# Optimization experiments

Hardware: AMD Instinct MI355X
Metric: run time of the kernel (lower is better)

## Reference

```python
import jax, jax.numpy as jnp
import numpy as np

D_IN, D_SAE, T, K = 768, 12288, 64, 64
B = 32


def setup_inputs() -> dict:
    key = jax.random.key(0)
    ks = jax.random.split(key, 4)
    x = jax.random.normal(ks[0], (B, T, D_IN), dtype=jnp.float32)
    W_enc = jax.random.normal(ks[1], (D_IN, D_SAE), dtype=jnp.float32) * (1.0 / D_IN ** 0.5)
    W_dec = jax.random.normal(ks[2], (D_SAE, D_IN), dtype=jnp.float32) * (1.0 / D_SAE ** 0.5)
    b_enc = jnp.zeros((D_SAE,), dtype=jnp.float32)
    b_dec = jnp.zeros((D_IN,), dtype=jnp.float32)
    gate_raw = jnp.zeros((D_SAE,), dtype=jnp.float32)  # gate_init = 0.0 -> sigmoid = 0.5
    return {"x": x, "W_enc": W_enc, "W_dec": W_dec, "b_enc": b_enc,
            "b_dec": b_dec, "gate_raw": gate_raw}


def _topk(pre, k):
    # pre: (B, d_sae) -> sparse (B, d_sae) keeping relu of top-k values per row
    v, i = jax.lax.top_k(pre, k)                      # (B, k)
    z = jnp.zeros_like(pre)
    rows = jnp.arange(pre.shape[0])[:, None]
    return z.at[rows, i].set(jax.nn.relu(v))


def reference(x, W_enc, W_dec, b_enc, b_dec, gate_raw):
    gate = jax.nn.sigmoid(gate_raw)                    # (d_sae,)
    pre_input = jnp.einsum('btd,ds->bts', x, W_enc) + b_enc  # (B, T, d_sae)

    z0 = _topk(pre_input[:, 0, :], K)                  # (B, d_sae)

    def step(z_prev, pre_t):
        z_t = _topk(gate * z_prev + pre_t, K)
        return z_t, z_t

    pre_rest = jnp.swapaxes(pre_input[:, 1:, :], 0, 1)  # (T-1, B, d_sae)
    _, zs = jax.lax.scan(step, z0, pre_rest)            # (T-1, B, d_sae)
    z_seq = jnp.concatenate([z0[:, None, :], jnp.swapaxes(zs, 0, 1)], axis=1)  # (B, T, d_sae)

    x_hat = jnp.einsum('bts,sd->btd', z_seq, W_dec) + b_dec  # (B, T, d_in)
    recon_loss = jnp.mean(jnp.sum((x_hat - x) ** 2, axis=-1))
    return recon_loss, x_hat, z_seq[:, -1, :]
```

## Files before the change

kernel.cpp:

```cpp
#include <hip/hip_runtime.h>
#include <hip/hip_bf16.h>
#include <math.h>

#define D_IN   768
#define D_SAE  12288
#define T_LEN  64
#define K_TOP  64
#define B_SZ   32
#define NROWS  (B_SZ * T_LEN)
#define KT     24

typedef _Float16 h8 __attribute__((ext_vector_type(8)));
typedef float f4 __attribute__((ext_vector_type(4)));

__device__ __forceinline__ unsigned int f2key(float f) {
  unsigned int u = __float_as_uint(f);
  return (u & 0x80000000u) ? ~u : (u | 0x80000000u);
}

__device__ __forceinline__ void barL() {
  __builtin_amdgcn_sched_barrier(0);
  asm volatile("s_waitcnt lgkmcnt(0)" ::: "memory");
  __builtin_amdgcn_s_barrier();
  __builtin_amdgcn_sched_barrier(0);
}

#define GLOAD16(g, l)                                                        \
  __builtin_amdgcn_global_load_lds(                                          \
      (const __attribute__((address_space(1))) unsigned int*)(g),            \
      (__attribute__((address_space(3))) unsigned int*)(l), 16, 0, 0)

__global__ void sae_init_out(float* __restrict__ d_out) {
  int i = blockIdx.x * blockDim.x + threadIdx.x;
  if (i == 0) d_out[0] = 0.0f;
  if (i < B_SZ * D_SAE) d_out[1 + (size_t)NROWS * D_IN + i] = 0.0f;
}

__global__ __launch_bounds__(256) void sae_split_A(
    const float* __restrict__ A, _Float16* __restrict__ Ah, _Float16* __restrict__ Al) {
  int g = blockIdx.x * 256 + threadIdx.x;
  int tile = g >> 6, l = g & 63;
  int tm = tile / KT, tk = tile - tm * KT;
  int m = (tm << 4) + (l & 15);
  int k = (tk << 5) + ((l >> 4) << 3);
  const float* src = A + (size_t)m * D_IN + k;
  float4 v0 = *(const float4*)src;
  float4 v1 = *(const float4*)(src + 4);
  float f[8] = {v0.x, v0.y, v0.z, v0.w, v1.x, v1.y, v1.z, v1.w};
  h8 hi, lo;
#pragma unroll
  for (int j = 0; j < 8; ++j) {
    _Float16 h = (_Float16)f[j];
    hi[j] = h;
    lo[j] = (_Float16)((f[j] - (float)h) * 4096.0f);
  }
  *(h8*)(Ah + (size_t)g * 8) = hi;
  *(h8*)(Al + (size_t)g * 8) = lo;
}

__global__ __launch_bounds__(256) void sae_split_B(
    const float* __restrict__ B, _Float16* __restrict__ Bh, _Float16* __restrict__ Bl) {
  int g = blockIdx.x * 256 + threadIdx.x;
  int tile = g >> 6, l = g & 63;
  int tn = tile / KT, tk = tile - tn * KT;
  int n = (tn << 4) + (l & 15);
  int k = (tk << 5) + ((l >> 4) << 3);
  h8 hi, lo;
#pragma unroll
  for (int j = 0; j < 8; ++j) {
    float f = B[(size_t)(k + j) * D_SAE + n];
    _Float16 h = (_Float16)f;
    hi[j] = h;
    lo[j] = (_Float16)((f - (float)h) * 4096.0f);
  }
  *(h8*)(Bh + (size_t)g * 8) = hi;
  *(h8*)(Bl + (size_t)g * 8) = lo;
}

__global__ __launch_bounds__(512) void sae_gemm_mfma(
    const _Float16* __restrict__ Ah, const _Float16* __restrict__ Al,
    const _Float16* __restrict__ Bh, const _Float16* __restrict__ Bl,
    const float* __restrict__ bias, float* __restrict__ C) {
  __shared__ _Float16 lds[2][16384];
  const int tid = threadIdx.x;
  const int w = tid >> 6, lane = tid & 63;
  const int wm = w >> 2, wn = w & 3;
  const int bmT = blockIdx.y * 8;
  const int bnT = blockIdx.x * 8;

  f4 accm[4][2], accc[4][2];
#pragma unroll
  for (int i = 0; i < 4; ++i)
#pragma unroll
    for (int j = 0; j < 2; ++j) {
      accm[i][j] = (f4){0.f, 0.f, 0.f, 0.f};
      accc[i][j] = (f4){0.f, 0.f, 0.f, 0.f};
    }

#define STAGE(buf, tk)                                                         \
  {                                                                            \
    const _Float16* s0 = Ah + ((size_t)(bmT + w) * KT + (tk)) * 512;           \
    const _Float16* s1 = Al + ((size_t)(bmT + w) * KT + (tk)) * 512;           \
    const _Float16* s2 = Bh + ((size_t)(bnT + w) * KT + (tk)) * 512;           \
    const _Float16* s3 = Bl + ((size_t)(bnT + w) * KT + (tk)) * 512;           \
    GLOAD16(s0 + lane * 8, &lds[buf][(0 * 8 + w) * 512]);                      \
    GLOAD16(s1 + lane * 8, &lds[buf][(1 * 8 + w) * 512]);                      \
    GLOAD16(s2 + lane * 8, &lds[buf][(2 * 8 + w) * 512]);                      \
    GLOAD16(s3 + lane * 8, &lds[buf][(3 * 8 + w) * 512]);                      \
  }

  STAGE(0, 0);
  __syncthreads();
  for (int tk = 0; tk < KT; ++tk) {
    int buf = tk & 1;
    if (tk + 1 < KT) STAGE(buf ^ 1, tk + 1);
    h8 ah[4], al4[4], bh2[2], bl2[2];
#pragma unroll
    for (int i = 0; i < 4; ++i) {
      ah[i]  = *(const h8*)&lds[buf][(wm * 4 + i) * 512 + lane * 8];
      al4[i] = *(const h8*)&lds[buf][4096 + (wm * 4 + i) * 512 + lane * 8];
    }
#pragma unroll
    for (int j = 0; j < 2; ++j) {
      bh2[j] = *(const h8*)&lds[buf][8192 + (wn * 2 + j) * 512 + lane * 8];
      bl2[j] = *(const h8*)&lds[buf][12288 + (wn * 2 + j) * 512 + lane * 8];
    }
#pragma unroll
    for (int i = 0; i < 4; ++i)
#pragma unroll
      for (int j = 0; j < 2; ++j) {
        accm[i][j] = __builtin_amdgcn_mfma_f32_16x16x32_f16(ah[i], bh2[j], accm[i][j], 0, 0, 0);
        accc[i][j] = __builtin_amdgcn_mfma_f32_16x16x32_f16(ah[i], bl2[j], accc[i][j], 0, 0, 0);
        accc[i][j] = __builtin_amdgcn_mfma_f32_16x16x32_f16(al4[i], bh2[j], accc[i][j], 0, 0, 0);
      }
    __syncthreads();
  }
#undef STAGE

  const float kLo = 1.0f / 4096.0f;
  const int colb = blockIdx.x * 128 + wn * 32;
  const int rowb = blockIdx.y * 128 + wm * 64;
#pragma unroll
  for (int j = 0; j < 2; ++j) {
    int col = colb + j * 16 + (lane & 15);
    float bv = bias[col];
#pragma unroll
    for (int i = 0; i < 4; ++i) {
      int row = rowb + i * 16 + ((lane >> 4) << 2);
#pragma unroll
      for (int r = 0; r < 4; ++r)
        C[(size_t)(row + r) * D_SAE + col] = accm[i][j][r] + accc[i][j][r] * kLo + bv;
    }
  }
}

__global__ __launch_bounds__(256) void sae_top128(
    const float* __restrict__ pre, int* __restrict__ t128i, float* __restrict__ t128v) {
  const int row = blockIdx.x;
  const int tid = threadIdx.x;
  __shared__ unsigned int keys[D_SAE];
  __shared__ int hist[256];
  __shared__ int scn[256];
  __shared__ int sb, srem, scnt, scnt2;
  const float* p = pre + (size_t)row * D_SAE;
  for (int i = tid; i < D_SAE; i += 256) keys[i] = f2key(p[i]);

  const unsigned int PMASK[4] = {0u, 0xFF000000u, 0xFFFF0000u, 0xFFFFFF00u};
  unsigned int pacc = 0;
  int remaining = 128;

  for (int round = 0; round < 4; ++round) {
    const int shift = 24 - 8 * round;
    hist[tid] = 0;
    __syncthreads();
    unsigned int pm = PMASK[round];
    for (int i = tid; i < D_SAE; i += 256) {
      unsigned int k = keys[i];
      if ((k & pm) == pacc) atomicAdd(&hist[(k >> shift) & 255], 1);
    }
    __syncthreads();
    scn[tid] = hist[tid];
    __syncthreads();
    for (int d = 1; d < 256; d <<= 1) {
      int nv = scn[tid] + ((tid + d < 256) ? scn[tid + d] : 0);
      __syncthreads();
      scn[tid] = nv;
      __syncthreads();
    }
    int cum = scn[tid];
    int nxt = (tid < 255) ? scn[tid + 1] : 0;
    if (cum >= remaining && nxt < remaining) { sb = tid; srem = remaining - nxt; }
    __syncthreads();
    pacc |= ((unsigned int)sb) << shift;
    remaining = srem;
    __syncthreads();
  }
  if (tid == 0) { scnt = 0; scnt2 = 0; }
  __syncthreads();
  const int ngt = 128 - remaining;
  for (int i = tid; i < D_SAE; i += 256) {
    unsigned int k = keys[i];
    if (k > pacc) {
      int pos = atomicAdd(&scnt, 1);
      t128i[row * 128 + pos] = i;
      t128v[row * 128 + pos] = p[i];
    } else if (k == pacc) {
      int pos = atomicAdd(&scnt2, 1);
      if (pos < remaining) {
        t128i[row * 128 + ngt + pos] = i;
        t128v[row * 128 + ngt + pos] = p[i];
      }
    }
  }
}

__global__ __launch_bounds__(256) void sae_recur(
    const float* __restrict__ pre, const int* __restrict__ t128i,
    const float* __restrict__ t128v, const float* __restrict__ gate_raw,
    int* __restrict__ zi, float* __restrict__ zv) {
  const int b = blockIdx.x;
  const int tid = threadIdx.x;
  const int lane = tid & 63;
  const int w = tid >> 6;
  __shared__ float prerow[D_SAE];
  __shared__ float boost[D_SAE];
  __shared__ float sgate[D_SAE];
  __shared__ unsigned char mark[D_SAE];
  __shared__ __align__(16) unsigned long long ckey[192];
  __shared__ int   szi[64];
  __shared__ float szv[64];
  __shared__ float szg[64];

  for (int i = tid; i < D_SAE; i += 256) {
    boost[i] = 0.0f;
    mark[i] = 0xFFu;
    sgate[i] = 1.0f / (1.0f + __expf(-gate_raw[i]));
  }
  if (tid < 64) { szi[tid] = tid; szv[tid] = 0.0f; szg[tid] = 0.0f; }
  {
    const float4* src = (const float4*)(pre + (size_t)(b * T_LEN) * D_SAE);
#pragma unroll
    for (int i = 0; i < 12; ++i) {
      float4 v = src[i * 256 + tid];
      *(float4*)&prerow[(size_t)(i * 256 + tid) * 4] = v;
    }
  }
  int ri = 0; float rv = 0.0f;
  if (tid < 128) {
    ri = t128i[(size_t)(b * T_LEN) * 128 + tid];
    rv = t128v[(size_t)(b * T_LEN) * 128 + tid];
  }
  __syncthreads();

  const unsigned long long lt64 = (1ull << lane) - 1ull;
  int zidx = 0; float zval = 0.0f, gz = 0.0f, pv = 0.0f;

  for (int t = 0; t < T_LEN; ++t) {
    const int row = b * T_LEN + t;
    if (w == 0) {
      zidx = szi[lane]; zval = szv[lane]; gz = szg[lane];
      if (zval > 0.0f) boost[zidx] = gz;
      pv = prerow[zidx];
    }
    if (tid < 128) mark[ri] = (unsigned char)t;
    barL();
    unsigned long long kc = 0;
    float myv = 0.0f; int myi = 0;
    if (tid < 128) {
      myi = ri;
      myv = rv + boost[ri];
      kc = (((unsigned long long)f2key(myv)) << 14) | (unsigned)(16383 - myi);
      ckey[tid] = kc;
    }
    if (w == 0) {
      bool active = (zval > 0.0f);
      bool matched = active && (mark[zidx] == (unsigned char)t);
      bool extra = active && !matched;
      unsigned long long em = __ballot(extra);
      int ne = __popcll(em);
      if (extra) {
        int pos = __popcll(em & lt64);
        float v = pv + gz;
        ckey[128 + pos] =
            (((unsigned long long)f2key(v)) << 14) | (unsigned)(16383 - zidx);
      }
      if (lane >= ne) {
        ckey[128 + lane] = (((unsigned long long)f2key(-INFINITY)) << 14) |
                           (unsigned)(16383 - (D_SAE + lane));
      }
    }
    barL();
    int nri = ri; float nrv = rv;
    if (tid < 128 && t + 1 < T_LEN) {
      nri = t128i[(size_t)(row + 1) * 128 + tid];
      nrv = t128v[(size_t)(row + 1) * 128 + tid];
    }
    if (w == 3) {
      if (t + 1 < T_LEN) {
        const float* src = pre + (size_t)(row + 1) * D_SAE + lane * 4;
#pragma unroll
        for (int i = 0; i < 48; ++i)
          GLOAD16(src + i * 256, &prerow[i * 256]);
      }
      int oz = szi[lane];
      boost[oz] = 0.0f;
    }
    if (tid >= 128 && tid < 192) {
      kc = ckey[tid];
      myi = 16383 - (int)(kc & 0x3FFFu);
      unsigned int hv = (unsigned int)(kc >> 14);
      myv = (hv & 0x80000000u) ? __uint_as_float(hv & 0x7FFFFFFFu)
                               : __uint_as_float(~hv);
    }
    int r = 0;
    if (tid < 192) {
#pragma unroll 8
      for (int j = 0; j < 96; ++j) {
        ulonglong2 kk = *(const ulonglong2*)&ckey[2 * j];
        r += (int)(kk.x > kc) + (int)(kk.y > kc);
      }
    }
    barL();
    if (tid < 192 && r < K_TOP) {
      float rl = fmaxf(myv, 0.0f);
      szi[r] = myi;
      szv[r] = rl;
      szg[r] = (rl > 0.0f) ? rl * sgate[myi] : 0.0f;
      zi[(size_t)row * 64 + r] = myi;
      zv[(size_t)row * 64 + r] = rl;
    }
    if (w == 3) {
      asm volatile("s_waitcnt vmcnt(0)" ::: "memory");
    }
    barL();
    ri = nri; rv = nrv;
  }
}

__global__ __launch_bounds__(256) void sae_decode(
    const float* __restrict__ x, const float* __restrict__ W_dec,
    const float* __restrict__ b_dec, const int* __restrict__ zi,
    const float* __restrict__ zv, float* __restrict__ d_out) {
  const int row = blockIdx.x;
  const int tid = threadIdx.x;
  __shared__ int   si[64];
  __shared__ float sv[64];
  __shared__ float red[4];
  if (tid < 64) { si[tid] = zi[row * 64 + tid]; sv[tid] = zv[row * 64 + tid]; }
  __syncthreads();
  float a0 = b_dec[tid], a1 = b_dec[tid + 256], a2 = b_dec[tid + 512];
  for (int k = 0; k < 64; ++k) {
    float v = sv[k];
    if (v != 0.0f) {
      const float* wp = W_dec + (size_t)si[k] * D_IN;
      a0 = fmaf(v, wp[tid], a0);
      a1 = fmaf(v, wp[tid + 256], a1);
      a2 = fmaf(v, wp[tid + 512], a2);
    }
  }
  float* xhat = d_out + 1;
  size_t base = (size_t)row * D_IN;
  xhat[base + tid]       = a0;
  xhat[base + tid + 256] = a1;
  xhat[base + tid + 512] = a2;
  float d0 = a0 - x[base + tid];
  float d1 = a1 - x[base + tid + 256];
  float d2 = a2 - x[base + tid + 512];
  float s = d0 * d0 + d1 * d1 + d2 * d2;
  for (int o = 32; o > 0; o >>= 1) s += __shfl_down(s, o);
  if ((tid & 63) == 0) red[tid >> 6] = s;
  __syncthreads();
  if (tid == 0) {
    float tot = red[0] + red[1] + red[2] + red[3];
    atomicAdd(d_out, tot * (1.0f / (float)NROWS));
  }
}

__global__ void sae_scatter_last(const int* __restrict__ zi,
                                 const float* __restrict__ zv,
                                 float* __restrict__ d_out) {
  int i = blockIdx.x * blockDim.x + threadIdx.x;
  if (i >= B_SZ * 64) return;
  int b = i >> 6, k = i & 63;
  int row = b * T_LEN + (T_LEN - 1);
  float* zlast = d_out + 1 + (size_t)NROWS * D_IN;
  zlast[(size_t)b * D_SAE + zi[row * 64 + k]] = zv[row * 64 + k];
}

extern "C" void kernel_launch(void* const* d_in, const int* in_sizes, int n_in,
                              void* d_out, int out_size, void* d_ws, size_t ws_size,
                              hipStream_t stream) {
  const float* x        = (const float*)d_in[0];
  const float* W_enc    = (const float*)d_in[1];
  const float* W_dec    = (const float*)d_in[2];
  const float* b_enc    = (const float*)d_in[3];
  const float* b_dec    = (const float*)d_in[4];
  const float* gate_raw = (const float*)d_in[5];
  float* out = (float*)d_out;

  char* ws = (char*)d_ws;
  size_t off = 0;
  float* pre   = (float*)(ws + off); off += (size_t)NROWS * D_SAE * sizeof(float);
  int*   t128i = (int*)(ws + off);   off += (size_t)NROWS * 128 * sizeof(int);
  float* t128v = (float*)(ws + off); off += (size_t)NROWS * 128 * sizeof(float);
  int*   zidx  = (int*)(ws + off);   off += (size_t)NROWS * 64 * sizeof(int);
  float* zval  = (float*)(ws + off); off += (size_t)NROWS * 64 * sizeof(float);
  _Float16* Ah = (_Float16*)(ws + off); off += (size_t)NROWS * D_IN * sizeof(_Float16);
  _Float16* Al = (_Float16*)(ws + off); off += (size_t)NROWS * D_IN * sizeof(_Float16);
  _Float16* Bh = (_Float16*)(ws + off); off += (size_t)D_IN * D_SAE * sizeof(_Float16);
  _Float16* Bl = (_Float16*)(ws + off); off += (size_t)D_IN * D_SAE * sizeof(_Float16);

  sae_init_out<<<(B_SZ * D_SAE + 255) / 256, 256, 0, stream>>>(out);
  sae_split_A<<<(NROWS * D_IN / 8 + 255) / 256, 256, 0, stream>>>(x, Ah, Al);
  sae_split_B<<<(D_IN * D_SAE / 8 + 255) / 256, 256, 0, stream>>>(W_enc, Bh, Bl);
  sae_gemm_mfma<<<dim3(D_SAE / 128, NROWS / 128), 512, 0, stream>>>(
      Ah, Al, Bh, Bl, b_enc, pre);
  sae_top128<<<NROWS, 256, 0, stream>>>(pre, t128i, t128v);
  sae_recur<<<B_SZ, 256, 0, stream>>>(pre, t128i, t128v, gate_raw, zidx, zval);
  sae_decode<<<NROWS, 256, 0, stream>>>(x, W_dec, b_dec, zidx, zval, out);
  sae_scatter_last<<<8, 256, 0, stream>>>(zidx, zval, out);
}
```

Baseline: 743.9 us.

## Double-buffer pre rows and trim rank loop to live candidates

Holds two pre-activation rows in shared memory and prefetches the row two steps ahead, waiting only on the older load batch, so global loads overlap more of the recurrent step. The rank loop covers only the live candidate count rather than a fixed 192, and one barrier is removed by writing results right after ranking. The per-feature sigmoid gate table is dropped in favour of computing the sigmoid on the fly for selected features. This uses more LDS, which may lower occupancy, and the partial vmcnt wait together with the removed barrier need careful ordering to avoid races on szi.

```diff
diff --git a/kernel.cpp b/kernel.cpp
--- a/kernel.cpp
+++ b/kernel.cpp
@@ -222,19 +222,18 @@
   const int tid = threadIdx.x;
   const int lane = tid & 63;
   const int w = tid >> 6;
-  __shared__ float prerow[D_SAE];
+  __shared__ float prerow[2][D_SAE];
   __shared__ float boost[D_SAE];
-  __shared__ float sgate[D_SAE];
   __shared__ unsigned char mark[D_SAE];
   __shared__ __align__(16) unsigned long long ckey[192];
   __shared__ int   szi[64];
   __shared__ float szv[64];
   __shared__ float szg[64];
+  __shared__ int   sne;
 
   for (int i = tid; i < D_SAE; i += 256) {
     boost[i] = 0.0f;
     mark[i] = 0xFFu;
-    sgate[i] = 1.0f / (1.0f + __expf(-gate_raw[i]));
   }
   if (tid < 64) { szi[tid] = tid; szv[tid] = 0.0f; szg[tid] = 0.0f; }
   {
@@ -242,26 +241,35 @@
 #pragma unroll
     for (int i = 0; i < 12; ++i) {
       float4 v = src[i * 256 + tid];
-      *(float4*)&prerow[(size_t)(i * 256 + tid) * 4] = v;
-    }
+      *(float4*)&prerow[0][(size_t)(i * 256 + tid) * 4] = v;
+    }
+  }
+  if (w == 3) {
+    const float* src1 = pre + (size_t)(b * T_LEN + 1) * D_SAE + lane * 4;
+#pragma unroll
+    for (int i = 0; i < 48; ++i)
+      GLOAD16(src1 + i * 256, &prerow[1][i * 256]);
   }
   int ri = 0; float rv = 0.0f;
   if (tid < 128) {
     ri = t128i[(size_t)(b * T_LEN) * 128 + tid];
     rv = t128v[(size_t)(b * T_LEN) * 128 + tid];
   }
-  __syncthreads();
+  barL();
 
   const unsigned long long lt64 = (1ull << lane) - 1ull;
   int zidx = 0; float zval = 0.0f, gz = 0.0f, pv = 0.0f;
+  int oz = 0;
 
   for (int t = 0; t < T_LEN; ++t) {
     const int row = b * T_LEN + t;
+    const int dbuf = t & 1;
     if (w == 0) {
       zidx = szi[lane]; zval = szv[lane]; gz = szg[lane];
       if (zval > 0.0f) boost[zidx] = gz;
-      pv = prerow[zidx];
-    }
+      pv = prerow[dbuf][zidx];
+    }
+    if (w == 3) oz = szi[lane];
     if (tid < 128) mark[ri] = (unsigned char)t;
     barL();
     unsigned long long kc = 0;
@@ -284,28 +292,33 @@
         ckey[128 + pos] =
             (((unsigned long long)f2key(v)) << 14) | (unsigned)(16383 - zidx);
       }
-      if (lane >= ne) {
-        ckey[128 + lane] = (((unsigned long long)f2key(-INFINITY)) << 14) |
-                           (unsigned)(16383 - (D_SAE + lane));
-      }
+      if (lane == ne) {
+        ckey[128 + ne] = (((unsigned long long)f2key(-INFINITY)) << 14) |
+                         (unsigned)(16383 - (D_SAE + ne));
+      }
+      if (lane == 0) sne = ne;
     }
     barL();
+    const int nk = 128 + sne;
     int nri = ri; float nrv = rv;
     if (tid < 128 && t + 1 < T_LEN) {
       nri = t128i[(size_t)(row + 1) * 128 + tid];
       nrv = t128v[(size_t)(row + 1) * 128 + tid];
     }
     if (w == 3) {
-      if (t + 1 < T_LEN) {
-        const float* src = pre + (size_t)(row + 1) * D_SAE + lane * 4;
-#pragma unroll
-        for (int i = 0; i < 48; ++i)
-          GLOAD16(src + i * 256, &prerow[i * 256]);
-      }
-      int oz = szi[lane];
+      const int last = b * T_LEN + T_LEN - 1;
+      const int nrow = (row + 2 <= last) ? row + 2 : last;
+      const float* src = pre + (size_t)nrow * D_SAE + lane * 4;
+      float* dst = &prerow[dbuf][0];
+#pragma unroll
+      for (int i = 0; i < 48; ++i)
+        GLOAD16(src + i * 256, dst + i * 256);
       boost[oz] = 0.0f;
-    }
-    if (tid >= 128 && tid < 192) {
+      __builtin_amdgcn_sched_barrier(0);
+      asm volatile("s_waitcnt vmcnt(48)" ::: "memory");
+      __builtin_amdgcn_sched_barrier(0);
+    }
+    if (tid >= 128 && tid < nk) {
       kc = ckey[tid];
       myi = 16383 - (int)(kc & 0x3FFFu);
       unsigned int hv = (unsigned int)(kc >> 14);
@@ -313,24 +326,23 @@
                                : __uint_as_float(~hv);
     }
     int r = 0;
-    if (tid < 192) {
+    if (tid < nk) {
+      const int np = (nk + 1) >> 1;
 #pragma unroll 8
-      for (int j = 0; j < 96; ++j) {
+      for (int j = 0; j < np; ++j) {
         ulonglong2 kk = *(const ulonglong2*)&ckey[2 * j];
         r += (int)(kk.x > kc) + (int)(kk.y > kc);
       }
-    }
-    barL();
-    if (tid < 192 && r < K_TOP) {
-      float rl = fmaxf(myv, 0.0f);
-      szi[r] = myi;
-      szv[r] = rl;
-      szg[r] = (rl > 0.0f) ? rl * sgate[myi] : 0.0f;
-      zi[(size_t)row * 64 + r] = myi;
-      zv[(size_t)row * 64 + r] = rl;
-    }
-    if (w == 3) {
-      asm volatile("s_waitcnt vmcnt(0)" ::: "memory");
+      if (r < K_TOP) {
+        float rl = fmaxf(myv, 0.0f);
+        float g = gate_raw[myi];
+        float s = 1.0f / (1.0f + __expf(-g));
+        szi[r] = myi;
+        szv[r] = rl;
+        szg[r] = rl * s;
+        zi[(size_t)row * 64 + r] = myi;
+        zv[(size_t)row * 64 + r] = rl;
+      }
     }
     barL();
     ri = nri; rv = nrv;
```

Result: faster. 653.3 us (-12.2%).
